# Performance work log

Hardware: AMD Instinct MI355X
Metric: run time of the kernel (lower is better)

The kernel has to match this reference:

```python
import jax, jax.numpy as jnp
import numpy as np
import math

IN_CH = 512
OUT_CH = 512
K = 3
STYLE_DIM = 512
EPS = 1e-8


def setup_inputs() -> dict:
    key = jax.random.key(0)
    k1, k2, k3, k4 = jax.random.split(key, 4)
    x = jax.random.normal(k1, (16, IN_CH, 64, 64), dtype=jnp.float32)
    style = jax.random.normal(k2, (16, STYLE_DIM), dtype=jnp.float32)
    weight = jax.random.normal(k3, (OUT_CH, IN_CH, K, K), dtype=jnp.float32)
    affine_w = jax.random.normal(k4, (IN_CH, STYLE_DIM), dtype=jnp.float32)
    affine_b = jnp.ones((IN_CH,), dtype=jnp.float32)  # bias_init=1.0
    return {"x": x, "style": style, "weight": weight,
            "affine_w": affine_w, "affine_b": affine_b}


def reference(x, style, weight, affine_w, affine_b):
    # EqualizedLinear: weight_scale = 1/sqrt(style_dim), lr_multiplier = 1
    w_scale = 1.0 / math.sqrt(STYLE_DIM)
    s = style @ (affine_w * w_scale).T + affine_b  # [B, Ci]

    # Demodulation factor: sigma_inv[b,o] = rsqrt(sum_{i,k,k} (w[o,i,k,k]*s[b,i])^2 + eps)
    wsq = jnp.sum(weight ** 2, axis=(2, 3))               # [Co, Ci]
    sigma_inv = jax.lax.rsqrt(jnp.einsum('oi,bi->bo', wsq, s ** 2) + EPS)  # [B, Co]

    # Modulated grouped conv == scale input per-channel, shared-weight conv,
    # scale output per-channel (conv is linear in the weight).
    x_mod = x * s[:, :, None, None]                        # [B, Ci, H, W]
    pad = K // 2
    y = jax.lax.conv_general_dilated(
        x_mod, weight,
        window_strides=(1, 1),
        padding=((pad, pad), (pad, pad)),
        dimension_numbers=('NCHW', 'OIHW', 'NCHW'))       # [B, Co, H, W]
    y = y * sigma_inv[:, :, None, None]
    return y
```

## Files before the change

### kernel.cpp

```cpp
#include <hip/hip_runtime.h>
#include <hip/hip_bf16.h>

#define BATCH 16
#define CI    512
#define CO    512
#define IMG   64
#define HP    66
#define NPIX  4096
#define NTAP  9

typedef __bf16  bf16x8  __attribute__((ext_vector_type(8)));
typedef float   floatx4 __attribute__((ext_vector_type(4)));

#define OFF_S     0u
#define OFF_SIG   32768u
#define OFF_WSQ   65536u
#define OFF_WBF   1114112u
#define OFF_XPAD  5832704u
#define XPAD_BYTES 71368704u
#define WS_NEEDED (OFF_XPAD + XPAD_BYTES)

__global__ void k_style(const float* __restrict__ style, const float* __restrict__ aw,
                        const float* __restrict__ ab, float* __restrict__ s_out)
{
    __shared__ float st[512];
    int b = blockIdx.x;
    int t = threadIdx.x;
    st[t]       = style[b * 512 + t];
    st[t + 256] = style[b * 512 + t + 256];
    __syncthreads();
    int i = blockIdx.y * 256 + t;
    const float4* awr = (const float4*)(aw + (size_t)i * 512);
    float sum = 0.f;
#pragma unroll 8
    for (int k = 0; k < 128; ++k) {
        float4 v = awr[k];
        sum += v.x * st[4 * k] + v.y * st[4 * k + 1] + v.z * st[4 * k + 2] + v.w * st[4 * k + 3];
    }
    s_out[b * 512 + i] = sum * 0.04419417382415922f + ab[i];
}

__global__ void k_wprep(const float* __restrict__ wgt, float* __restrict__ wsq,
                        unsigned short* __restrict__ wbf)
{
    int idx = blockIdx.x * 256 + threadIdx.x;
    const float* p = wgt + (size_t)idx * 9;
    float q = 0.f;
#pragma unroll
    for (int t9 = 0; t9 < 9; ++t9) {
        float v = p[t9];
        q += v * v;
        __hip_bfloat16 hv = __float2bfloat16(v);
        wbf[t9 * 262144 + idx] = *(unsigned short*)&hv;
    }
    wsq[idx] = q;
}

__global__ void k_sigma(const float* __restrict__ s_in, const float* __restrict__ wsq,
                        float* __restrict__ sig)
{
    __shared__ float s2[512];
    int b = blockIdx.x, t = threadIdx.x;
    float a0 = s_in[b * 512 + t], a1 = s_in[b * 512 + t + 256];
    s2[t] = a0 * a0;
    s2[t + 256] = a1 * a1;
    __syncthreads();
    int o = blockIdx.y * 256 + t;
    const float4* wr = (const float4*)(wsq + (size_t)o * 512);
    float sum = 0.f;
#pragma unroll 8
    for (int k = 0; k < 128; ++k) {
        float4 v = wr[k];
        sum += v.x * s2[4 * k] + v.y * s2[4 * k + 1] + v.z * s2[4 * k + 2] + v.w * s2[4 * k + 3];
    }
    sig[b * 512 + o] = rsqrtf(sum + 1e-8f);
}

__global__ void k_halo(unsigned short* __restrict__ xpad)
{
    int b = blockIdx.x, p = blockIdx.y, t = threadIdx.x;
    int h, w;
    if (p < 66)       { h = 0;            w = p; }
    else if (p < 132) { h = 65;           w = p - 66; }
    else if (p < 196) { h = 1 + (p - 132); w = 0; }
    else              { h = 1 + (p - 196); w = 65; }
    unsigned int* dst = (unsigned int*)(xpad + ((size_t)((b * 66 + h) * 66 + w)) * 512);
    dst[t] = 0u;
}

__global__ void k_xmod(const float* __restrict__ x, const float* __restrict__ s_in,
                       unsigned short* __restrict__ xpad)
{
    __shared__ unsigned short tile[64 * 256];
    __shared__ float sm_s[256];
    int b = blockIdx.x, h = blockIdx.y, half = blockIdx.z;
    int ci0 = half * 256;
    int t = threadIdx.x;

    sm_s[t] = s_in[b * 512 + ci0 + t];
    __syncthreads();

    int w0 = (t & 15) * 4;
    int cp = (t >> 4) * 2;
#pragma unroll
    for (int i = 0; i < 8; ++i) {
        int ci_l = i * 32 + cp;
        float sv0 = sm_s[ci_l], sv1 = sm_s[ci_l + 1];
        const float4 v0 = *(const float4*)(x + (((size_t)(b * 512 + ci0 + ci_l)) << 12) + (h << 6) + w0);
        const float4 v1 = *(const float4*)(x + (((size_t)(b * 512 + ci0 + ci_l + 1)) << 12) + (h << 6) + w0);
        float a0[4] = {v0.x, v0.y, v0.z, v0.w};
        float a1[4] = {v1.x, v1.y, v1.z, v1.w};
#pragma unroll
        for (int j = 0; j < 4; ++j) {
            int w = w0 + j;
            __hip_bfloat16 h0 = __float2bfloat16(a0[j] * sv0);
            __hip_bfloat16 h1 = __float2bfloat16(a1[j] * sv1);
            unsigned int packed = (unsigned int)(*(unsigned short*)&h0)
                                | ((unsigned int)(*(unsigned short*)&h1) << 16);
            int off = w * 256 + (((ci_l >> 3) ^ ((w >> 2) & 7)) << 3) + (ci_l & 7);
            *(unsigned int*)&tile[off] = packed;
        }
    }
    __syncthreads();

    int q = t & 31;
#pragma unroll
    for (int i = 0; i < 8; ++i) {
        int w = i * 8 + (t >> 5);
        int off = w * 256 + ((q ^ ((w >> 2) & 7)) << 3);
        uint4 v = *(const uint4*)&tile[off];
        *(uint4*)(xpad + ((size_t)((b * 66 + h + 1) * 66 + (w + 1))) * 512 + ci0 + q * 8) = v;
    }
}

__device__ __forceinline__ void gload16(const void* g, void* l)
{
    __builtin_amdgcn_global_load_lds(
        (const __attribute__((address_space(1))) unsigned int*)g,
        (__attribute__((address_space(3))) unsigned int*)l, 16, 0, 0);
}

__global__ __launch_bounds__(256, 2)
void k_conv(const unsigned short* __restrict__ xpad, const unsigned short* __restrict__ wbf,
            const float* __restrict__ sig, float* __restrict__ y)
{
    __shared__ unsigned short A_lds[4096];
    __shared__ unsigned short B_lds[4096];
    int t = threadIdx.x;
    int w = t >> 6, l = t & 63;
    int wr = w >> 1, wc = w & 1;
    int bx = blockIdx.x;
    int b = bx >> 7, rem = bx & 127;
    int co_t = rem >> 5, pix_t = rem & 31;
    int o_base = co_t << 7;
    int h0 = pix_t << 1;

    const char* wb = (const char*)wbf;
    const char* xb = (const char*)xpad;

    int idx0 = (w << 6) + l;
    int idx1 = idx0 + 256;
    int sw = (((idx0 & 3) ^ ((idx0 >> 3) & 3)) << 4);
    int aoff0 = ((o_base + (idx0 >> 2)) << 10) + sw;
    int aoff1 = ((o_base + (idx1 >> 2)) << 10) + sw;
    int p0 = idx0 >> 2, p1 = idx1 >> 2;
    int boff0 = (((b * 66 + h0 + (p0 >> 6)) * 66 + (p0 & 63)) << 10) + sw;
    int boff1 = (((b * 66 + h0 + (p1 >> 6)) * 66 + (p1 & 63)) << 10) + sw;
    char* aL0 = (char*)A_lds + (w << 10);
    char* aL1 = (char*)A_lds + 4096 + (w << 10);
    char* bL0 = (char*)B_lds + (w << 10);
    char* bL1 = (char*)B_lds + 4096 + (w << 10);

    floatx4 acc[4][4];
#pragma unroll
    for (int i = 0; i < 4; ++i)
#pragma unroll
        for (int j = 0; j < 4; ++j)
            acc[i][j] = (floatx4){0.f, 0.f, 0.f, 0.f};

    int lr = l & 15;
    int fsw = (((l >> 4) ^ ((lr >> 1) & 3)) << 3);
    int fa = wr * 2048 + lr * 32 + fsw;
    int fb = wc * 2048 + lr * 32 + fsw;

    for (int tap = 0; tap < 9; ++tap) {
        int kh = tap / 3;
        int kw = tap - kh * 3;
        int tb = (kh * 66 + kw) << 10;
        int ta = tap << 19;
        for (int cic = 0; cic < 16; ++cic) {
            int kb = cic << 6;
            gload16(wb + ta + kb + aoff0, aL0);
            gload16(wb + ta + kb + aoff1, aL1);
            gload16(xb + tb + kb + boff0, bL0);
            gload16(xb + tb + kb + boff1, bL1);
            __syncthreads();

            bf16x8 af[4], bfr[4];
#pragma unroll
            for (int i = 0; i < 4; ++i) af[i]  = *(const bf16x8*)&A_lds[fa + i * 512];
#pragma unroll
            for (int j = 0; j < 4; ++j) bfr[j] = *(const bf16x8*)&B_lds[fb + j * 512];
#pragma unroll
            for (int i = 0; i < 4; ++i)
#pragma unroll
                for (int j = 0; j < 4; ++j)
                    acc[i][j] = __builtin_amdgcn_mfma_f32_16x16x32_bf16(af[i], bfr[j], acc[i][j], 0, 0, 0);
            __syncthreads();
        }
    }

    int col = l & 15, quad = l >> 4;
    const float* sb = sig + b * 512;
#pragma unroll
    for (int i = 0; i < 4; ++i) {
        int ob = o_base + wr * 64 + i * 16 + quad * 4;
#pragma unroll
        for (int r = 0; r < 4; ++r) {
            int o = ob + r;
            float sv = sb[o];
            float* yrow = y + (((size_t)(b * 512 + o)) << 12);
#pragma unroll
            for (int j = 0; j < 4; ++j) {
                int pix = (pix_t << 7) + wc * 64 + j * 16 + col;
                yrow[pix] = acc[i][j][r] * sv;
            }
        }
    }
}

extern "C" void kernel_launch(void* const* d_in, const int* in_sizes, int n_in,
                              void* d_out, int out_size, void* d_ws, size_t ws_size,
                              hipStream_t stream)
{
    const float* x        = (const float*)d_in[0];
    const float* style    = (const float*)d_in[1];
    const float* weight   = (const float*)d_in[2];
    const float* affine_w = (const float*)d_in[3];
    const float* affine_b = (const float*)d_in[4];
    float* y = (float*)d_out;

    if (ws_size < (size_t)WS_NEEDED) return;

    char* ws = (char*)d_ws;
    float*          s_buf = (float*)(ws + OFF_S);
    float*          sig   = (float*)(ws + OFF_SIG);
    float*          wsq   = (float*)(ws + OFF_WSQ);
    unsigned short* wbf   = (unsigned short*)(ws + OFF_WBF);
    unsigned short* xpad  = (unsigned short*)(ws + OFF_XPAD);

    k_halo<<<dim3(16, 260), 256, 0, stream>>>(xpad);
    k_style<<<dim3(16, 2), 256, 0, stream>>>(style, affine_w, affine_b, s_buf);
    k_wprep<<<1024, 256, 0, stream>>>(weight, wsq, wbf);
    k_sigma<<<dim3(16, 2), 256, 0, stream>>>(s_buf, wsq, sig);
    k_xmod<<<dim3(16, 64, 2), 256, 0, stream>>>(x, s_buf, xpad);
    k_conv<<<2048, 256, 0, stream>>>(xpad, wbf, sig, y);
}
```

Baseline: 639.7 us.

## Share one input tile across three horizontal taps in conv loop

The conv kernel now loads a 2-row by 66-pixel input strip once per kh and channel chunk, and reads it at three column offsets for the kw taps. Weights for all three kw taps are staged together, which triples A LDS. This removes redundant input global loads and cuts barriers per MFMA by a factor of three. Separately, the halo-zeroing kernel is folded into the x-modulation kernel, which now uses 128-channel quarters, and the launch order is shuffled. The larger LDS footprint may reduce occupancy.

Result: faster. 560.3 us (-12.4%).

```diff
diff --git a/kernel.cpp b/kernel.cpp
--- a/kernel.cpp
+++ b/kernel.cpp
@@ -76,60 +76,62 @@
     sig[b * 512 + o] = rsqrtf(sum + 1e-8f);
 }
 
-__global__ void k_halo(unsigned short* __restrict__ xpad)
-{
-    int b = blockIdx.x, p = blockIdx.y, t = threadIdx.x;
-    int h, w;
-    if (p < 66)       { h = 0;            w = p; }
-    else if (p < 132) { h = 65;           w = p - 66; }
-    else if (p < 196) { h = 1 + (p - 132); w = 0; }
-    else              { h = 1 + (p - 196); w = 65; }
-    unsigned int* dst = (unsigned int*)(xpad + ((size_t)((b * 66 + h) * 66 + w)) * 512);
-    dst[t] = 0u;
-}
-
 __global__ void k_xmod(const float* __restrict__ x, const float* __restrict__ s_in,
                        unsigned short* __restrict__ xpad)
 {
-    __shared__ unsigned short tile[64 * 256];
-    __shared__ float sm_s[256];
-    int b = blockIdx.x, h = blockIdx.y, half = blockIdx.z;
-    int ci0 = half * 256;
+    __shared__ unsigned short tile[64 * 128];
+    __shared__ float sm_s[128];
+    int b = blockIdx.x, h = blockIdx.y, quarter = blockIdx.z;
+    int ci0 = quarter << 7;
     int t = threadIdx.x;
-
-    sm_s[t] = s_in[b * 512 + ci0 + t];
-    __syncthreads();
-
-    int w0 = (t & 15) * 4;
-    int cp = (t >> 4) * 2;
-#pragma unroll
-    for (int i = 0; i < 8; ++i) {
-        int ci_l = i * 32 + cp;
-        float sv0 = sm_s[ci_l], sv1 = sm_s[ci_l + 1];
-        const float4 v0 = *(const float4*)(x + (((size_t)(b * 512 + ci0 + ci_l)) << 12) + (h << 6) + w0);
-        const float4 v1 = *(const float4*)(x + (((size_t)(b * 512 + ci0 + ci_l + 1)) << 12) + (h << 6) + w0);
+    if (t < 128) sm_s[t] = s_in[b * 512 + ci0 + t];
+    __syncthreads();
+
+    int w0 = (t & 15) << 2;
+    int cp = (t >> 4) << 1;
+#pragma unroll
+    for (int i = 0; i < 4; ++i) {
+        int cl = (i << 5) + cp;
+        float sv0 = sm_s[cl], sv1 = sm_s[cl + 1];
+        float4 v0 = *(const float4*)(x + (((size_t)(b * 512 + ci0 + cl)) << 12) + (h << 6) + w0);
+        float4 v1 = *(const float4*)(x + (((size_t)(b * 512 + ci0 + cl + 1)) << 12) + (h << 6) + w0);
         float a0[4] = {v0.x, v0.y, v0.z, v0.w};
         float a1[4] = {v1.x, v1.y, v1.z, v1.w};
 #pragma unroll
         for (int j = 0; j < 4; ++j) {
-            int w = w0 + j;
+            int wq = w0 + j;
             __hip_bfloat16 h0 = __float2bfloat16(a0[j] * sv0);
             __hip_bfloat16 h1 = __float2bfloat16(a1[j] * sv1);
             unsigned int packed = (unsigned int)(*(unsigned short*)&h0)
                                 | ((unsigned int)(*(unsigned short*)&h1) << 16);
-            int off = w * 256 + (((ci_l >> 3) ^ ((w >> 2) & 7)) << 3) + (ci_l & 7);
+            int off = (wq << 7) + ((((cl >> 3) ^ ((wq >> 2) & 7))) << 3) + (cl & 7);
             *(unsigned int*)&tile[off] = packed;
         }
     }
     __syncthreads();
 
-    int q = t & 31;
-#pragma unroll
-    for (int i = 0; i < 8; ++i) {
-        int w = i * 8 + (t >> 5);
-        int off = w * 256 + ((q ^ ((w >> 2) & 7)) << 3);
+    int q = t & 15;
+    size_t rowb = (size_t)((b * 66 + h + 1) * 66 + 1) * 512 + ci0;
+#pragma unroll
+    for (int i = 0; i < 4; ++i) {
+        int wq = (i << 4) + (t >> 4);
+        int off = (wq << 7) + ((q ^ ((wq >> 2) & 7)) << 3);
         uint4 v = *(const uint4*)&tile[off];
-        *(uint4*)(xpad + ((size_t)((b * 66 + h + 1) * 66 + (w + 1))) * 512 + ci0 + q * 8) = v;
+        *(uint4*)(xpad + rowb + (size_t)wq * 512 + (q << 3)) = v;
+    }
+
+    uint4 z = {0u, 0u, 0u, 0u};
+    if (t < 32) {
+        int wp = (t >> 4) * 65;
+        *(uint4*)(xpad + (size_t)((b * 66 + h + 1) * 66 + wp) * 512 + ci0 + ((t & 15) << 3)) = z;
+    }
+    if (h == 0 || h == 63) {
+        int hp = (h == 0) ? 0 : 65;
+        size_t base = (size_t)(b * 66 + hp) * 66 * 512 + ci0;
+        for (int idx = t; idx < 66 * 16; idx += 256) {
+            int p = idx >> 4, c = idx & 15;
+            *(uint4*)(xpad + base + (size_t)p * 512 + (c << 3)) = z;
+        }
     }
 }
 
@@ -144,8 +146,8 @@
 void k_conv(const unsigned short* __restrict__ xpad, const unsigned short* __restrict__ wbf,
             const float* __restrict__ sig, float* __restrict__ y)
 {
-    __shared__ unsigned short A_lds[4096];
-    __shared__ unsigned short B_lds[4096];
+    __shared__ unsigned short A_lds[3 * 4096];
+    __shared__ unsigned short B_lds[4224];
     int t = threadIdx.x;
     int w = t >> 6, l = t & 63;
     int wr = w >> 1, wc = w & 1;
@@ -160,16 +162,42 @@
 
     int idx0 = (w << 6) + l;
     int idx1 = idx0 + 256;
-    int sw = (((idx0 & 3) ^ ((idx0 >> 3) & 3)) << 4);
-    int aoff0 = ((o_base + (idx0 >> 2)) << 10) + sw;
-    int aoff1 = ((o_base + (idx1 >> 2)) << 10) + sw;
-    int p0 = idx0 >> 2, p1 = idx1 >> 2;
-    int boff0 = (((b * 66 + h0 + (p0 >> 6)) * 66 + (p0 & 63)) << 10) + sw;
-    int boff1 = (((b * 66 + h0 + (p1 >> 6)) * 66 + (p1 & 63)) << 10) + sw;
-    char* aL0 = (char*)A_lds + (w << 10);
-    char* aL1 = (char*)A_lds + 4096 + (w << 10);
-    char* bL0 = (char*)B_lds + (w << 10);
-    char* bL1 = (char*)B_lds + 4096 + (w << 10);
+    int asw = (((idx0 & 3) ^ ((idx0 >> 3) & 3)) << 4);
+    int aof0 = ((o_base + (idx0 >> 2)) << 10) + asw;
+    int aof1 = aof0 + 65536;
+
+    int r0 = idx0 >> 2;
+    int bof0 = ((b * 66 + h0) * 66 + r0) * 1024 + (((idx0 & 3) ^ ((r0 >> 1) & 3)) << 4);
+    int r1 = idx1 >> 2;
+    int sr1 = (r1 >= 66) ? 1 : 0;
+    int wp1 = r1 - 66 * sr1;
+    int bof1 = ((b * 66 + h0 + sr1) * 66 + wp1) * 1024 + (((idx1 & 3) ^ ((r1 >> 1) & 3)) << 4);
+    int idxt = 512 + (w << 2) + l;
+    int rt = 128 + w;
+    int boft = ((b * 66 + h0 + 1) * 66 + 62 + w) * 1024 + (((idxt & 3) ^ ((rt >> 1) & 3)) << 4);
+
+    char* aldsb = (char*)A_lds;
+    char* bldsb = (char*)B_lds;
+    char* aL00 = aldsb + (w << 10);
+    char* aL01 = aldsb + 4096 + (w << 10);
+    char* aL10 = aldsb + 8192 + (w << 10);
+    char* aL11 = aldsb + 12288 + (w << 10);
+    char* aL20 = aldsb + 16384 + (w << 10);
+    char* aL21 = aldsb + 20480 + (w << 10);
+    char* bL0 = bldsb + (w << 10);
+    char* bL1 = bldsb + 4096 + (w << 10);
+    char* bLt = bldsb + ((512 + (w << 2)) << 4);
+
+    int lr = l & 15, q = l >> 4;
+    int fa = wr * 2048 + lr * 32 + ((q ^ ((lr >> 1) & 3)) << 3);
+    int fbo[3][4];
+#pragma unroll
+    for (int kw = 0; kw < 3; ++kw)
+#pragma unroll
+        for (int j = 0; j < 4; ++j) {
+            int sp = wc * 66 + j * 16 + lr + kw;
+            fbo[kw][j] = sp * 32 + ((q ^ ((sp >> 1) & 3)) << 3);
+        }
 
     floatx4 acc[4][4];
 #pragma unroll
@@ -178,34 +206,37 @@
         for (int j = 0; j < 4; ++j)
             acc[i][j] = (floatx4){0.f, 0.f, 0.f, 0.f};
 
-    int lr = l & 15;
-    int fsw = (((l >> 4) ^ ((lr >> 1) & 3)) << 3);
-    int fa = wr * 2048 + lr * 32 + fsw;
-    int fb = wc * 2048 + lr * 32 + fsw;
-
-    for (int tap = 0; tap < 9; ++tap) {
-        int kh = tap / 3;
-        int kw = tap - kh * 3;
-        int tb = (kh * 66 + kw) << 10;
-        int ta = tap << 19;
+    for (int kh = 0; kh < 3; ++kh) {
+        const char* wkh = wb + kh * 1572864;
+        const char* xkh = xb + kh * 67584;
         for (int cic = 0; cic < 16; ++cic) {
             int kb = cic << 6;
-            gload16(wb + ta + kb + aoff0, aL0);
-            gload16(wb + ta + kb + aoff1, aL1);
-            gload16(xb + tb + kb + boff0, bL0);
-            gload16(xb + tb + kb + boff1, bL1);
+            const char* wk = wkh + kb;
+            const char* xk = xkh + kb;
+            gload16(wk + aof0,           aL00);
+            gload16(wk + aof1,           aL01);
+            gload16(wk + 524288 + aof0,  aL10);
+            gload16(wk + 524288 + aof1,  aL11);
+            gload16(wk + 1048576 + aof0, aL20);
+            gload16(wk + 1048576 + aof1, aL21);
+            gload16(xk + bof0, bL0);
+            gload16(xk + bof1, bL1);
+            if (l < 4) gload16(xk + boft, bLt);
             __syncthreads();
 
-            bf16x8 af[4], bfr[4];
-#pragma unroll
-            for (int i = 0; i < 4; ++i) af[i]  = *(const bf16x8*)&A_lds[fa + i * 512];
-#pragma unroll
-            for (int j = 0; j < 4; ++j) bfr[j] = *(const bf16x8*)&B_lds[fb + j * 512];
-#pragma unroll
-            for (int i = 0; i < 4; ++i)
-#pragma unroll
-                for (int j = 0; j < 4; ++j)
-                    acc[i][j] = __builtin_amdgcn_mfma_f32_16x16x32_bf16(af[i], bfr[j], acc[i][j], 0, 0, 0);
+#pragma unroll
+            for (int kw = 0; kw < 3; ++kw) {
+                bf16x8 bfr[4], af[4];
+#pragma unroll
+                for (int j = 0; j < 4; ++j) bfr[j] = *(const bf16x8*)&B_lds[fbo[kw][j]];
+#pragma unroll
+                for (int i = 0; i < 4; ++i) af[i]  = *(const bf16x8*)&A_lds[kw * 4096 + fa + i * 512];
+#pragma unroll
+                for (int i = 0; i < 4; ++i)
+#pragma unroll
+                    for (int j = 0; j < 4; ++j)
+                        acc[i][j] = __builtin_amdgcn_mfma_f32_16x16x32_bf16(af[i], bfr[j], acc[i][j], 0, 0, 0);
+            }
             __syncthreads();
         }
     }
@@ -249,10 +280,9 @@
     unsigned short* wbf   = (unsigned short*)(ws + OFF_WBF);
     unsigned short* xpad  = (unsigned short*)(ws + OFF_XPAD);
 
-    k_halo<<<dim3(16, 260), 256, 0, stream>>>(xpad);
     k_style<<<dim3(16, 2), 256, 0, stream>>>(style, affine_w, affine_b, s_buf);
     k_wprep<<<1024, 256, 0, stream>>>(weight, wsq, wbf);
+    k_xmod<<<dim3(16, 64, 4), 256, 0, stream>>>(x, s_buf, xpad);
     k_sigma<<<dim3(16, 2), 256, 0, stream>>>(s_buf, wsq, sig);
-    k_xmod<<<dim3(16, 64, 2), 256, 0, stream>>>(x, s_buf, xpad);
     k_conv<<<2048, 256, 0, stream>>>(xpad, wbf, sig, y);
 }
```
